# Kernel optimization log

Measured on AMD Instinct MI355X. Metric: run time of the kernel, lower is better.

Reference implementation:

```python
import jax, jax.numpy as jnp
import numpy as np

N, F = 400000, 128
M = 100000
DENSE = [256, 256, 128]


def setup_inputs() -> dict:
    key = jax.random.key(0)
    ks = jax.random.split(key, 8)
    x = jax.random.normal(ks[0], (N, F), dtype=jnp.float32)
    sel_idx = jax.random.randint(ks[1], (M, 1), 0, N, dtype=jnp.int32)
    # Dense layer params, scaled like glorot-ish init
    W0 = jax.random.normal(ks[2], (F, DENSE[0]), dtype=jnp.float32) * (1.0 / np.sqrt(F))
    b0 = jnp.zeros((DENSE[0],), dtype=jnp.float32)
    W1 = jax.random.normal(ks[3], (DENSE[0], DENSE[1]), dtype=jnp.float32) * (1.0 / np.sqrt(DENSE[0]))
    b1 = jnp.zeros((DENSE[1],), dtype=jnp.float32)
    W2 = jax.random.normal(ks[4], (DENSE[1], DENSE[2]), dtype=jnp.float32) * (1.0 / np.sqrt(DENSE[1]))
    b2 = jnp.zeros((DENSE[2],), dtype=jnp.float32)
    return {"x": x, "sel_idx": sel_idx, "W0": W0, "b0": b0,
            "W1": W1, "b1": b1, "W2": W2, "b2": b2}


def reference(x, sel_idx, W0, b0, W1, b1, W2, b2):
    idx = sel_idx[:, 0]                       # [M]
    up = x[idx]                               # gather_nd -> [M, F]
    up = jax.nn.elu(up @ W0 + b0)             # [M, 256]
    up = jax.nn.elu(up @ W1 + b1)             # [M, 256]
    up = jax.nn.elu(up @ W2 + b2)             # [M, F]
    # x += scatter_nd(sel_idx, up, shape(x))
    return x + jnp.zeros_like(x).at[idx].add(up)
```

## Files before the change

kernel.cpp:

```cpp
#include <hip/hip_runtime.h>
#include <hip/hip_bf16.h>

#define NROWS 400000
#define MSEL  100000
#define FDIM  128
#define D0 256
#define D1 256
#define D2 128

typedef __attribute__((ext_vector_type(8))) short short8;
typedef __attribute__((ext_vector_type(4))) float f32x4;
typedef __attribute__((ext_vector_type(4))) unsigned short ushort4v;
typedef __attribute__((ext_vector_type(2))) unsigned int uint2v;

__device__ __forceinline__ unsigned short f2bf(float f) {
    unsigned int u = __float_as_uint(f);
    unsigned int r = (u + 0x7fffu + ((u >> 16) & 1u)) >> 16;
    return (unsigned short)r;
}

__device__ __forceinline__ unsigned int pk2bf(float a, float b) {
    __hip_bfloat162 h = __float22bfloat162_rn(make_float2(a, b));
    return *(unsigned int*)&h;
}

__device__ __forceinline__ float elu(float v) {
    return v > 0.f ? v : (__expf(v) - 1.f);
}

__global__ void pack_weights(const float* __restrict__ W0,
                             const float* __restrict__ W1,
                             const float* __restrict__ W2,
                             short* __restrict__ out) {
    int e = blockIdx.x * 256 + threadIdx.x;
    if (e >= 131072) return;
    const float* W; int N; int base; int le;
    if (e < 32768)       { W = W0; N = 256; base = 0;     le = e; }
    else if (e < 98304)  { W = W1; N = 256; base = 32768; le = e - 32768; }
    else                 { W = W2; N = 128; base = 98304; le = e - 98304; }
    int t    = le >> 9;
    int r    = le & 511;
    int lane = r >> 3;
    int j    = r & 7;
    int ntiles = N >> 4;
    int kt = t / ntiles, nt = t % ntiles;
    int k = kt * 32 + (lane >> 4) * 8 + j;
    int n = nt * 16 + (lane & 15);
    out[base + le] = (short)f2bf(W[k * N + n]);
}

__global__ void copy_x(const float4* __restrict__ x, float4* __restrict__ out, int n4) {
    int i = blockIdx.x * blockDim.x + threadIdx.x;
    int stride = gridDim.x * blockDim.x;
    for (; i < n4; i += stride) out[i] = x[i];
}

__global__ void init_head(int* __restrict__ head) {
    int i = blockIdx.x * 256 + threadIdx.x;
    int s = gridDim.x * 256;
    for (; i < NROWS; i += s) head[i] = -1;
}

__global__ void build_links(const int* __restrict__ sel,
                            int* __restrict__ head, int* __restrict__ next) {
    int j = blockIdx.x * 256 + threadIdx.x;
    if (j < MSEL) {
        int r = sel[j];
        next[j] = atomicExch(head + r, j);
    }
}

template <bool SPLIT>
__global__ __launch_bounds__(256) void mlp_fused(
    const float* __restrict__ x, const int* __restrict__ sel,
    const short* __restrict__ wp,
    const float* __restrict__ b0v, const float* __restrict__ b1v,
    const float* __restrict__ b2v,
    unsigned short* __restrict__ upOut, float* __restrict__ out) {
    __shared__ __align__(16) short lds[16384];

    const int tid  = threadIdx.x;
    const int lane = tid & 63;
    const int w    = tid >> 6;
    const int rowBase = blockIdx.x * 32;
    const int lm = lane & 15;
    const int kq = lane >> 4;
    const int sxz = (lm & 7) << 3;

    const short* W0p = wp;
    const short* W1p = wp + 32768;
    const short* W2p = wp + 98304;

    const float4* xs = (const float4*)x + (size_t)blockIdx.x * 4096;
    float4* os = (float4*)out + (size_t)blockIdx.x * 4096;
    float4 cc0, cc1, cc2, cc3;
#define LOADC(c)  { int b_ = (c) * 1024 + tid; cc0 = xs[b_]; cc1 = xs[b_ + 256]; \
                    cc2 = xs[b_ + 512]; cc3 = xs[b_ + 768]; }
#define STOREC(c) { int b_ = (c) * 1024 + tid; os[b_] = cc0; os[b_ + 256] = cc1; \
                    os[b_ + 512] = cc2; os[b_ + 768] = cc3; }

    short8 B0[4][4];
    #pragma unroll
    for (int kt = 0; kt < 4; kt++)
        #pragma unroll
        for (int ntl = 0; ntl < 4; ntl++)
            B0[kt][ntl] = *(const short8*)(W0p + ((kt * 16 + (w * 4 + ntl)) * 512 + lane * 8));

    const float4* xv = (const float4*)x;
    #pragma unroll
    for (int it = 0; it < 4; it++) {
        int i = it * 256 + tid;
        int row = i >> 5, seg = i & 31;
        float4 v = xv[(size_t)sel[rowBase + row] * 32 + seg];
        uint2v p = { pk2bf(v.x, v.y), pk2bf(v.z, v.w) };
        *(uint2v*)(&lds[(row * 128 + seg * 4) ^ ((row & 7) << 3)]) = p;
    }
    __syncthreads();

    if (SPLIT) LOADC(0);

    const f32x4 zero4 = {0.f, 0.f, 0.f, 0.f};

    {
        f32x4 acc[2][4];
        #pragma unroll
        for (int i = 0; i < 2; i++)
            #pragma unroll
            for (int j = 0; j < 4; j++) acc[i][j] = zero4;
        #pragma unroll
        for (int rt = 0; rt < 2; rt++) {
            short8 a[4];
            int rowA = rt * 16 + lm;
            #pragma unroll
            for (int kt = 0; kt < 4; kt++)
                a[kt] = *(const short8*)(&lds[(rowA * 128 + kt * 32 + kq * 8) ^ sxz]);
            #pragma unroll
            for (int ntl = 0; ntl < 4; ntl++)
                #pragma unroll
                for (int kt = 0; kt < 4; kt++)
                    acc[rt][ntl] = __builtin_amdgcn_mfma_f32_16x16x32_bf16(a[kt], B0[kt][ntl], acc[rt][ntl], 0, 0, 0);
        }
        #pragma unroll
        for (int ntl = 0; ntl < 4; ntl++) {
            int col = (w * 4 + ntl) * 16 + lm;
            float bias = b0v[col];
            #pragma unroll
            for (int rt = 0; rt < 2; rt++) {
                float v0 = elu(acc[rt][ntl][0] + bias);
                float v1 = elu(acc[rt][ntl][1] + bias);
                float v2 = elu(acc[rt][ntl][2] + bias);
                float v3 = elu(acc[rt][ntl][3] + bias);
                unsigned int u01 = pk2bf(v0, v1), u23 = pk2bf(v2, v3);
                int row = rt * 16 + kq * 4;
                lds[4096 + (((row+0) * 256 + col) ^ (((row+0) & 7) << 3))] = (short)(u01 & 0xffff);
                lds[4096 + (((row+1) * 256 + col) ^ (((row+1) & 7) << 3))] = (short)(u01 >> 16);
                lds[4096 + (((row+2) * 256 + col) ^ (((row+2) & 7) << 3))] = (short)(u23 & 0xffff);
                lds[4096 + (((row+3) * 256 + col) ^ (((row+3) & 7) << 3))] = (short)(u23 >> 16);
            }
        }
    }
    __syncthreads();

    if (SPLIT) { STOREC(0); LOADC(1); }

    #pragma unroll
    for (int pass = 0; pass < 2; pass++) {
        short8 B1[8][2];
        #pragma unroll
        for (int kt = 0; kt < 8; kt++)
            #pragma unroll
            for (int p = 0; p < 2; p++)
                B1[kt][p] = *(const short8*)(W1p + ((kt * 16 + (w * 4 + pass * 2 + p)) * 512 + lane * 8));
        f32x4 acc[2][2];
        #pragma unroll
        for (int i = 0; i < 2; i++)
            #pragma unroll
            for (int j = 0; j < 2; j++) acc[i][j] = zero4;
        #pragma unroll
        for (int rt = 0; rt < 2; rt++) {
            short8 a[8];
            int rowA = rt * 16 + lm;
            #pragma unroll
            for (int kt = 0; kt < 8; kt++)
                a[kt] = *(const short8*)(&lds[4096 + ((rowA * 256 + kt * 32 + kq * 8) ^ sxz)]);
            #pragma unroll
            for (int p = 0; p < 2; p++)
                #pragma unroll
                for (int kt = 0; kt < 8; kt++)
                    acc[rt][p] = __builtin_amdgcn_mfma_f32_16x16x32_bf16(a[kt], B1[kt][p], acc[rt][p], 0, 0, 0);
        }
        #pragma unroll
        for (int p = 0; p < 2; p++) {
            int col = (w * 4 + pass * 2 + p) * 16 + lm;
            float bias = b1v[col];
            #pragma unroll
            for (int rt = 0; rt < 2; rt++) {
                float v0 = elu(acc[rt][p][0] + bias);
                float v1 = elu(acc[rt][p][1] + bias);
                float v2 = elu(acc[rt][p][2] + bias);
                float v3 = elu(acc[rt][p][3] + bias);
                unsigned int u01 = pk2bf(v0, v1), u23 = pk2bf(v2, v3);
                int row = rt * 16 + kq * 4;
                int hb = rt ? 0 : 12288;
                lds[hb + ((((row+0) & 15) * 256 + col) ^ (((row+0) & 7) << 3))] = (short)(u01 & 0xffff);
                lds[hb + ((((row+1) & 15) * 256 + col) ^ (((row+1) & 7) << 3))] = (short)(u01 >> 16);
                lds[hb + ((((row+2) & 15) * 256 + col) ^ (((row+2) & 7) << 3))] = (short)(u23 & 0xffff);
                lds[hb + ((((row+3) & 15) * 256 + col) ^ (((row+3) & 7) << 3))] = (short)(u23 >> 16);
            }
        }
        if (SPLIT && pass == 0) { STOREC(1); LOADC(2); }
    }
    __syncthreads();

    if (SPLIT) { STOREC(2); LOADC(3); }

    {
        short8 B2[8][2];
        #pragma unroll
        for (int kt = 0; kt < 8; kt++)
            #pragma unroll
            for (int ntl = 0; ntl < 2; ntl++)
                B2[kt][ntl] = *(const short8*)(W2p + ((kt * 8 + (w * 2 + ntl)) * 512 + lane * 8));

        f32x4 acc[2][2];
        #pragma unroll
        for (int i = 0; i < 2; i++)
            #pragma unroll
            for (int j = 0; j < 2; j++) acc[i][j] = zero4;
        #pragma unroll
        for (int rt = 0; rt < 2; rt++) {
            short8 a[8];
            int rowA = rt * 16 + lm;
            int hb = rt ? 0 : 12288;
            #pragma unroll
            for (int kt = 0; kt < 8; kt++)
                a[kt] = *(const short8*)(&lds[hb + (((rowA & 15) * 256 + kt * 32 + kq * 8) ^ sxz)]);
            #pragma unroll
            for (int ntl = 0; ntl < 2; ntl++)
                #pragma unroll
                for (int kt = 0; kt < 8; kt++)
                    acc[rt][ntl] = __builtin_amdgcn_mfma_f32_16x16x32_bf16(a[kt], B2[kt][ntl], acc[rt][ntl], 0, 0, 0);
        }
        #pragma unroll
        for (int ntl = 0; ntl < 2; ntl++) {
            int col = (w * 2 + ntl) * 16 + lm;
            float bias = b2v[col];
            #pragma unroll
            for (int rt = 0; rt < 2; rt++)
                #pragma unroll
                for (int r = 0; r < 4; r++) {
                    int row = rt * 16 + kq * 4 + r;
                    float v = elu(acc[rt][ntl][r] + bias);
                    if (SPLIT) {
                        lds[4096 + row * 128 + col] = (short)f2bf(v);
                    } else {
                        atomicAdd(out + (size_t)sel[rowBase + row] * 128 + col, v);
                    }
                }
        }
    }
    if (SPLIT) {
        __syncthreads();
        const short8* s8 = (const short8*)(&lds[4096]);
        short8* u8 = (short8*)(upOut + (size_t)rowBase * 128);
        u8[tid]       = s8[tid];
        u8[tid + 256] = s8[tid + 256];
        STOREC(3);
    }
#undef LOADC
#undef STOREC
}

__global__ __launch_bounds__(256) void merge_touched(
    const float2* __restrict__ x2, const unsigned int* __restrict__ up32,
    const int* __restrict__ head, const int* __restrict__ next,
    float2* __restrict__ out2) {
    int wid  = blockIdx.x * 4 + (threadIdx.x >> 6);
    int lane = threadIdx.x & 63;
    int wstride = gridDim.x * 4;
    for (int row = wid; row < NROWS; row += wstride) {
        int j = head[row];
        if (j < 0) continue;
        float2 v = x2[(size_t)row * 64 + lane];
        do {
            unsigned int u = up32[(size_t)j * 64 + lane];
            v.x += __uint_as_float(u << 16);
            v.y += __uint_as_float(u & 0xffff0000u);
            j = next[j];
        } while (j >= 0);
        out2[(size_t)row * 64 + lane] = v;
    }
}

extern "C" void kernel_launch(void* const* d_in, const int* in_sizes, int n_in,
                              void* d_out, int out_size, void* d_ws, size_t ws_size,
                              hipStream_t stream) {
    const float* x   = (const float*)d_in[0];
    const int*   sel = (const int*)d_in[1];
    const float* W0  = (const float*)d_in[2];
    const float* b0  = (const float*)d_in[3];
    const float* W1  = (const float*)d_in[4];
    const float* b1  = (const float*)d_in[5];
    const float* W2  = (const float*)d_in[6];
    const float* b2  = (const float*)d_in[7];
    float* out = (float*)d_out;

    char* wsb = (char*)d_ws;
    short* wp          = (short*)wsb;
    unsigned short* up = (unsigned short*)(wsb + 262144);
    int* head          = (int*)(wsb + 262144 + (size_t)MSEL * 256);
    int* nxt           = head + NROWS;
    const size_t need  = 262144 + (size_t)MSEL * 256 + (size_t)NROWS * 4 + (size_t)MSEL * 4;

    pack_weights<<<512, 256, 0, stream>>>(W0, W1, W2, wp);
    if (ws_size >= need) {
        init_head<<<1024, 256, 0, stream>>>(head);
        build_links<<<(MSEL + 255) / 256, 256, 0, stream>>>(sel, head, nxt);
        mlp_fused<true><<<MSEL / 32, 256, 0, stream>>>(x, sel, wp, b0, b1, b2, up, out);
        merge_touched<<<4096, 256, 0, stream>>>((const float2*)x, (const unsigned int*)up,
                                                head, nxt, (float2*)out);
    } else {
        copy_x<<<4096, 256, 0, stream>>>((const float4*)x, (float4*)out, NROWS * FDIM / 4);
        mlp_fused<false><<<MSEL / 32, 256, 0, stream>>>(x, sel, wp, b0, b1, b2, up, out);
    }
}
```

Before: 160.8 us.

## Move x copy into merge pass and prefetch weights across MLP layers

Drops the interleaved copy of the first M rows of x from the MLP kernel. The merge kernel now reads every row of x and writes every output row, so it handles the base copy for all rows rather than only the touched ones. The MLP kernel also issues the gather loads before the W0 fragment loads, and prefetches the W1 and W2 fragments one stage early so their latency overlaps MFMA work. The cost is more register pressure from holding extra weight fragments, plus a merge kernel that now streams the full x array.

```diff
diff --git a/kernel.cpp b/kernel.cpp
--- a/kernel.cpp
+++ b/kernel.cpp
@@ -71,7 +71,7 @@
 }
 
 template <bool SPLIT>
-__global__ __launch_bounds__(256) void mlp_fused(
+__global__ __launch_bounds__(256) void mlp_compute(
     const float* __restrict__ x, const int* __restrict__ sel,
     const short* __restrict__ wp,
     const float* __restrict__ b0v, const float* __restrict__ b1v,
@@ -91,13 +91,15 @@
     const short* W1p = wp + 32768;
     const short* W2p = wp + 98304;
 
-    const float4* xs = (const float4*)x + (size_t)blockIdx.x * 4096;
-    float4* os = (float4*)out + (size_t)blockIdx.x * 4096;
-    float4 cc0, cc1, cc2, cc3;
-#define LOADC(c)  { int b_ = (c) * 1024 + tid; cc0 = xs[b_]; cc1 = xs[b_ + 256]; \
-                    cc2 = xs[b_ + 512]; cc3 = xs[b_ + 768]; }
-#define STOREC(c) { int b_ = (c) * 1024 + tid; os[b_] = cc0; os[b_ + 256] = cc1; \
-                    os[b_ + 512] = cc2; os[b_ + 768] = cc3; }
+    const float4* xv = (const float4*)x;
+    float4 gv[4];
+    int grow[4], gseg[4];
+    #pragma unroll
+    for (int it = 0; it < 4; it++) {
+        int i = it * 256 + tid;
+        grow[it] = i >> 5; gseg[it] = i & 31;
+        gv[it] = xv[(size_t)sel[rowBase + grow[it]] * 32 + gseg[it]];
+    }
 
     short8 B0[4][4];
     #pragma unroll
@@ -106,21 +108,16 @@
         for (int ntl = 0; ntl < 4; ntl++)
             B0[kt][ntl] = *(const short8*)(W0p + ((kt * 16 + (w * 4 + ntl)) * 512 + lane * 8));
 
-    const float4* xv = (const float4*)x;
     #pragma unroll
     for (int it = 0; it < 4; it++) {
-        int i = it * 256 + tid;
-        int row = i >> 5, seg = i & 31;
-        float4 v = xv[(size_t)sel[rowBase + row] * 32 + seg];
-        uint2v p = { pk2bf(v.x, v.y), pk2bf(v.z, v.w) };
-        *(uint2v*)(&lds[(row * 128 + seg * 4) ^ ((row & 7) << 3)]) = p;
+        uint2v p = { pk2bf(gv[it].x, gv[it].y), pk2bf(gv[it].z, gv[it].w) };
+        *(uint2v*)(&lds[(grow[it] * 128 + gseg[it] * 4) ^ ((grow[it] & 7) << 3)]) = p;
     }
     __syncthreads();
 
-    if (SPLIT) LOADC(0);
-
     const f32x4 zero4 = {0.f, 0.f, 0.f, 0.f};
 
+    short8 B1a[8][2];
     {
         f32x4 acc[2][4];
         #pragma unroll
@@ -140,6 +137,12 @@
                 for (int kt = 0; kt < 4; kt++)
                     acc[rt][ntl] = __builtin_amdgcn_mfma_f32_16x16x32_bf16(a[kt], B0[kt][ntl], acc[rt][ntl], 0, 0, 0);
         }
+        #pragma unroll
+        for (int kt = 0; kt < 8; kt++)
+            #pragma unroll
+            for (int p = 0; p < 2; p++)
+                B1a[kt][p] = *(const short8*)(W1p + ((kt * 16 + (w * 4 + p)) * 512 + lane * 8));
+
         #pragma unroll
         for (int ntl = 0; ntl < 4; ntl++) {
             int col = (w * 4 + ntl) * 16 + lm;
@@ -161,16 +164,15 @@
     }
     __syncthreads();
 
-    if (SPLIT) { STOREC(0); LOADC(1); }
-
-    #pragma unroll
-    for (int pass = 0; pass < 2; pass++) {
-        short8 B1[8][2];
+    short8 B2[8][2];
+    {
+        short8 B1b[8][2];
         #pragma unroll
         for (int kt = 0; kt < 8; kt++)
             #pragma unroll
             for (int p = 0; p < 2; p++)
-                B1[kt][p] = *(const short8*)(W1p + ((kt * 16 + (w * 4 + pass * 2 + p)) * 512 + lane * 8));
+                B1b[kt][p] = *(const short8*)(W1p + ((kt * 16 + (w * 4 + 2 + p)) * 512 + lane * 8));
+
         f32x4 acc[2][2];
         #pragma unroll
         for (int i = 0; i < 2; i++)
@@ -187,11 +189,11 @@
             for (int p = 0; p < 2; p++)
                 #pragma unroll
                 for (int kt = 0; kt < 8; kt++)
-                    acc[rt][p] = __builtin_amdgcn_mfma_f32_16x16x32_bf16(a[kt], B1[kt][p], acc[rt][p], 0, 0, 0);
+                    acc[rt][p] = __builtin_amdgcn_mfma_f32_16x16x32_bf16(a[kt], B1a[kt][p], acc[rt][p], 0, 0, 0);
         }
         #pragma unroll
         for (int p = 0; p < 2; p++) {
-            int col = (w * 4 + pass * 2 + p) * 16 + lm;
+            int col = (w * 4 + p) * 16 + lm;
             float bias = b1v[col];
             #pragma unroll
             for (int rt = 0; rt < 2; rt++) {
@@ -208,20 +210,53 @@
                 lds[hb + ((((row+3) & 15) * 256 + col) ^ (((row+3) & 7) << 3))] = (short)(u23 >> 16);
             }
         }
-        if (SPLIT && pass == 0) { STOREC(1); LOADC(2); }
-    }
-    __syncthreads();
-
-    if (SPLIT) { STOREC(2); LOADC(3); }
-
-    {
-        short8 B2[8][2];
+
+        #pragma unroll
+        for (int i = 0; i < 2; i++)
+            #pragma unroll
+            for (int j = 0; j < 2; j++) acc[i][j] = zero4;
+        #pragma unroll
+        for (int rt = 0; rt < 2; rt++) {
+            short8 a[8];
+            int rowA = rt * 16 + lm;
+            #pragma unroll
+            for (int kt = 0; kt < 8; kt++)
+                a[kt] = *(const short8*)(&lds[4096 + ((rowA * 256 + kt * 32 + kq * 8) ^ sxz)]);
+            #pragma unroll
+            for (int p = 0; p < 2; p++)
+                #pragma unroll
+                for (int kt = 0; kt < 8; kt++)
+                    acc[rt][p] = __builtin_amdgcn_mfma_f32_16x16x32_bf16(a[kt], B1b[kt][p], acc[rt][p], 0, 0, 0);
+        }
         #pragma unroll
         for (int kt = 0; kt < 8; kt++)
             #pragma unroll
             for (int ntl = 0; ntl < 2; ntl++)
                 B2[kt][ntl] = *(const short8*)(W2p + ((kt * 8 + (w * 2 + ntl)) * 512 + lane * 8));
 
+        #pragma unroll
+        for (int p = 0; p < 2; p++) {
+            int col = (w * 4 + 2 + p) * 16 + lm;
+            float bias = b1v[col];
+            #pragma unroll
+            for (int rt = 0; rt < 2; rt++) {
+                float v0 = elu(acc[rt][p][0] + bias);
+                float v1 = elu(acc[rt][p][1] + bias);
+                float v2 = elu(acc[rt][p][2] + bias);
+                float v3 = elu(acc[rt][p][3] + bias);
+                unsigned int u01 = pk2bf(v0, v1), u23 = pk2bf(v2, v3);
+                int row = rt * 16 + kq * 4;
+                int hb = rt ? 0 : 12288;
+                lds[hb + ((((row+0) & 15) * 256 + col) ^ (((row+0) & 7) << 3))] = (short)(u01 & 0xffff);
+                lds[hb + ((((row+1) & 15) * 256 + col) ^ (((row+1) & 7) << 3))] = (short)(u01 >> 16);
+                lds[hb + ((((row+2) & 15) * 256 + col) ^ (((row+2) & 7) << 3))] = (short)(u23 & 0xffff);
+                lds[hb + ((((row+3) & 15) * 256 + col) ^ (((row+3) & 7) << 3))] = (short)(u23 >> 16);
+            }
+        }
+    }
+    __syncthreads();
+
+    {
         f32x4 acc[2][2];
         #pragma unroll
         for (int i = 0; i < 2; i++)
@@ -265,13 +300,10 @@
         short8* u8 = (short8*)(upOut + (size_t)rowBase * 128);
         u8[tid]       = s8[tid];
         u8[tid + 256] = s8[tid + 256];
-        STOREC(3);
-    }
-#undef LOADC
-#undef STOREC
-}
-
-__global__ __launch_bounds__(256) void merge_touched(
+    }
+}
+
+__global__ __launch_bounds__(256) void merge_out(
     const float2* __restrict__ x2, const unsigned int* __restrict__ up32,
     const int* __restrict__ head, const int* __restrict__ next,
     float2* __restrict__ out2) {
@@ -279,15 +311,14 @@
     int lane = threadIdx.x & 63;
     int wstride = gridDim.x * 4;
     for (int row = wid; row < NROWS; row += wstride) {
+        float2 v = x2[(size_t)row * 64 + lane];
         int j = head[row];
-        if (j < 0) continue;
-        float2 v = x2[(size_t)row * 64 + lane];
-        do {
+        while (j >= 0) {
             unsigned int u = up32[(size_t)j * 64 + lane];
             v.x += __uint_as_float(u << 16);
             v.y += __uint_as_float(u & 0xffff0000u);
             j = next[j];
-        } while (j >= 0);
+        }
         out2[(size_t)row * 64 + lane] = v;
     }
 }
@@ -316,11 +347,11 @@
     if (ws_size >= need) {
         init_head<<<1024, 256, 0, stream>>>(head);
         build_links<<<(MSEL + 255) / 256, 256, 0, stream>>>(sel, head, nxt);
-        mlp_fused<true><<<MSEL / 32, 256, 0, stream>>>(x, sel, wp, b0, b1, b2, up, out);
-        merge_touched<<<4096, 256, 0, stream>>>((const float2*)x, (const unsigned int*)up,
-                                                head, nxt, (float2*)out);
+        mlp_compute<true><<<MSEL / 32, 256, 0, stream>>>(x, sel, wp, b0, b1, b2, up, out);
+        merge_out<<<4096, 256, 0, stream>>>((const float2*)x, (const unsigned int*)up,
+                                            head, nxt, (float2*)out);
     } else {
         copy_x<<<4096, 256, 0, stream>>>((const float4*)x, (float4*)out, NROWS * FDIM / 4);
-        mlp_fused<false><<<MSEL / 32, 256, 0, stream>>>(x, sel, wp, b0, b1, b2, up, out);
-    }
-}
+        mlp_compute<false><<<MSEL / 32, 256, 0, stream>>>(x, sel, wp, b0, b1, b2, up, out);
+    }
+}
```

New measurement: 151.3 us. -5.9%, faster.

## Skip copy of touched rows, hoist gather loads, use LDS-only barriers

Applied to the files above, without the earlier changes.

The fused MLP kernel now reads the head array so it copies x to out only for rows that no selected index touches, since merge_touched rewrites those rows anyway. The gather loads are issued into registers before the weight loads, and the bf16 packing into LDS happens after the first x-copy chunk is loaded. __syncthreads is replaced by a barrier that waits only on LDS counters, so outstanding global loads and stores can stay in flight across phases. The trade-offs are extra head reads per chunk, divergent conditional stores, and more live registers.

```diff
diff --git a/kernel.cpp b/kernel.cpp
--- a/kernel.cpp
+++ b/kernel.cpp
@@ -26,6 +26,13 @@
 
 __device__ __forceinline__ float elu(float v) {
     return v > 0.f ? v : (__expf(v) - 1.f);
+}
+
+__device__ __forceinline__ void ldsbar() {
+    __builtin_amdgcn_sched_barrier(0);
+    asm volatile("s_waitcnt lgkmcnt(0)" ::: "memory");
+    __builtin_amdgcn_s_barrier();
+    __builtin_amdgcn_sched_barrier(0);
 }
 
 __global__ void pack_weights(const float* __restrict__ W0,
@@ -76,6 +83,7 @@
     const short* __restrict__ wp,
     const float* __restrict__ b0v, const float* __restrict__ b1v,
     const float* __restrict__ b2v,
+    const int* __restrict__ head,
     unsigned short* __restrict__ upOut, float* __restrict__ out) {
     __shared__ __align__(16) short lds[16384];
 
@@ -93,11 +101,26 @@
 
     const float4* xs = (const float4*)x + (size_t)blockIdx.x * 4096;
     float4* os = (float4*)out + (size_t)blockIdx.x * 4096;
+    const int hbase = blockIdx.x * 128;
     float4 cc0, cc1, cc2, cc3;
-#define LOADC(c)  { int b_ = (c) * 1024 + tid; cc0 = xs[b_]; cc1 = xs[b_ + 256]; \
-                    cc2 = xs[b_ + 512]; cc3 = xs[b_ + 768]; }
-#define STOREC(c) { int b_ = (c) * 1024 + tid; os[b_] = cc0; os[b_ + 256] = cc1; \
-                    os[b_ + 512] = cc2; os[b_ + 768] = cc3; }
+    int ch0, ch1, ch2, ch3;
+#define LOADC(c)  { int b_ = (c) * 1024 + tid; \
+                    cc0 = xs[b_]; cc1 = xs[b_ + 256]; cc2 = xs[b_ + 512]; cc3 = xs[b_ + 768]; \
+                    ch0 = head[hbase + (b_ >> 5)];        ch1 = head[hbase + ((b_ + 256) >> 5)]; \
+                    ch2 = head[hbase + ((b_ + 512) >> 5)]; ch3 = head[hbase + ((b_ + 768) >> 5)]; }
+#define STOREC(c) { int b_ = (c) * 1024 + tid; \
+                    if (ch0 < 0) os[b_]       = cc0; if (ch1 < 0) os[b_ + 256] = cc1; \
+                    if (ch2 < 0) os[b_ + 512] = cc2; if (ch3 < 0) os[b_ + 768] = cc3; }
+
+    const float4* xv = (const float4*)x;
+    float4 gv[4];
+    int grow[4], gseg[4];
+    #pragma unroll
+    for (int it = 0; it < 4; it++) {
+        int i = it * 256 + tid;
+        grow[it] = i >> 5; gseg[it] = i & 31;
+        gv[it] = xv[(size_t)sel[rowBase + grow[it]] * 32 + gseg[it]];
+    }
 
     short8 B0[4][4];
     #pragma unroll
@@ -106,18 +129,14 @@
         for (int ntl = 0; ntl < 4; ntl++)
             B0[kt][ntl] = *(const short8*)(W0p + ((kt * 16 + (w * 4 + ntl)) * 512 + lane * 8));
 
-    const float4* xv = (const float4*)x;
+    if (SPLIT) LOADC(0);
+
     #pragma unroll
     for (int it = 0; it < 4; it++) {
-        int i = it * 256 + tid;
-        int row = i >> 5, seg = i & 31;
-        float4 v = xv[(size_t)sel[rowBase + row] * 32 + seg];
-        uint2v p = { pk2bf(v.x, v.y), pk2bf(v.z, v.w) };
-        *(uint2v*)(&lds[(row * 128 + seg * 4) ^ ((row & 7) << 3)]) = p;
-    }
-    __syncthreads();
-
-    if (SPLIT) LOADC(0);
+        uint2v p = { pk2bf(gv[it].x, gv[it].y), pk2bf(gv[it].z, gv[it].w) };
+        *(uint2v*)(&lds[(grow[it] * 128 + gseg[it] * 4) ^ ((grow[it] & 7) << 3)]) = p;
+    }
+    ldsbar();
 
     const f32x4 zero4 = {0.f, 0.f, 0.f, 0.f};
 
@@ -159,7 +178,7 @@
             }
         }
     }
-    __syncthreads();
+    ldsbar();
 
     if (SPLIT) { STOREC(0); LOADC(1); }
 
@@ -210,7 +229,7 @@
         }
         if (SPLIT && pass == 0) { STOREC(1); LOADC(2); }
     }
-    __syncthreads();
+    ldsbar();
 
     if (SPLIT) { STOREC(2); LOADC(3); }
 
@@ -260,12 +279,12 @@
         }
     }
     if (SPLIT) {
-        __syncthreads();
+        STOREC(3);
+        ldsbar();
         const short8* s8 = (const short8*)(&lds[4096]);
         short8* u8 = (short8*)(upOut + (size_t)rowBase * 128);
         u8[tid]       = s8[tid];
         u8[tid + 256] = s8[tid + 256];
-        STOREC(3);
     }
 #undef LOADC
 #undef STOREC
@@ -316,11 +335,11 @@
     if (ws_size >= need) {
         init_head<<<1024, 256, 0, stream>>>(head);
         build_links<<<(MSEL + 255) / 256, 256, 0, stream>>>(sel, head, nxt);
-        mlp_fused<true><<<MSEL / 32, 256, 0, stream>>>(x, sel, wp, b0, b1, b2, up, out);
+        mlp_fused<true><<<MSEL / 32, 256, 0, stream>>>(x, sel, wp, b0, b1, b2, head, up, out);
         merge_touched<<<4096, 256, 0, stream>>>((const float2*)x, (const unsigned int*)up,
                                                 head, nxt, (float2*)out);
     } else {
         copy_x<<<4096, 256, 0, stream>>>((const float4*)x, (float4*)out, NROWS * FDIM / 4);
-        mlp_fused<false><<<MSEL / 32, 256, 0, stream>>>(x, sel, wp, b0, b1, b2, up, out);
-    }
-}
+        mlp_fused<false><<<MSEL / 32, 256, 0, stream>>>(x, sel, wp, b0, b1, b2, head, up, out);
+    }
+}
```

After: 175.5 us. 9.1% more time.
